# Kernel tuning notes

Measured on AMD Instinct MI355X. Metric: run time of the kernel, lower is better.

Reference implementation:

```python
import jax, jax.numpy as jnp
import numpy as np

DIM = 1792      # 256+512+1024 = WRN50 layer1-3 channels
GAMMA_D = 1
K_TOP = 3
EPS = 0.1
MAX_ITER = 200
B, H, W = 2, 56, 56


def avg_pool3x3(x):
    # F.avg_pool2d(x, 3, 1, 1), count_include_pad=True -> always divide by 9
    s = jax.lax.reduce_window(x, 0.0, jax.lax.add, (1, 1, 3, 3), (1, 1, 1, 1),
                              [(0, 0), (0, 0), (1, 1), (1, 1)])
    return s / 9.0


def descriptor(p1, p2, p3, w_coord, b_coord, w_eca):
    sample = avg_pool3x3(p1)
    b, _, h, w = sample.shape
    for o in (p2, p3):
        o = avg_pool3x3(o)
        # F.interpolate(..., mode='bilinear', align_corners=False) == half-pixel bilinear
        o = jax.image.resize(o, (o.shape[0], o.shape[1], h, w), method='bilinear')
        sample = jnp.concatenate([sample, o], axis=1)      # [b,1792,h,w]
    # CoordConv2d(dim, dim//gamma_d, 1): append normalized coord channels, 1x1 conv
    xx = jnp.broadcast_to(jnp.linspace(-1.0, 1.0, w, dtype=sample.dtype)[None, None, None, :], (b, 1, h, w))
    yy = jnp.broadcast_to(jnp.linspace(-1.0, 1.0, h, dtype=sample.dtype)[None, None, :, None], (b, 1, h, w))
    z = jnp.concatenate([sample, xx, yy], axis=1)          # [b,1794,h,w]
    phi = jnp.einsum('bchw,oc->bohw', z, w_coord) + b_coord[None, :, None, None]
    # eca_layer(dim, k_size=9): GAP -> conv1d over channel axis -> sigmoid gate
    y = phi.mean(axis=(2, 3))                              # [b,C]
    y = jax.lax.conv_general_dilated(y[:, None, :], w_eca[None, None, :], (1,),
                                     [(4, 4)], dimension_numbers=('NCH', 'OIH', 'NCH'))[:, 0, :]
    gate = jax.nn.sigmoid(y)[:, :, None, None]
    return phi * (1.0 + 0.1 * gate)                        # 0.1*eca(phi) + phi


def sinkhorn(Ccost, mu, nu):
    # plain Sinkhorn (TopK_custom forward), 200 iterations
    G = jnp.exp(-Ccost / EPS)                              # [bs,n,m]
    bs, n, m = Ccost.shape

    def body(i, uv):
        u, v = uv
        u = mu / (G * v).sum(-1, keepdims=True)            # [bs,n,1]
        v = nu / (G * u).sum(-2, keepdims=True)            # [bs,1,m]
        return (u, v)

    u0 = jnp.ones((bs, n, 1), Ccost.dtype)
    v0 = jnp.ones((bs, 1, m), Ccost.dtype) / m
    u, v = jax.lax.fori_loop(0, MAX_ITER, body, (u0, v0))
    return u * G * v


def soft_topk(scores):
    # SOFT top-k via 2-anchor optimal transport; selects the K_TOP SMALLEST scores
    bs, n = scores.shape
    anchors = jnp.array([0.0, 1.0], scores.dtype)          # [selected, rest]
    Ccost = (scores[..., None] - anchors) ** 2             # [bs,n,2]
    Ccost = Ccost / jax.lax.stop_gradient(Ccost.max())
    mu = jnp.ones((1, n, 1), scores.dtype) / n
    nu = jnp.array([K_TOP / n, (n - K_TOP) / n], scores.dtype).reshape(1, 1, 2)
    Gamma = sinkhorn(Ccost, mu, nu)
    return Gamma[..., 0] * n                               # soft top-K membership mask


def adfa_forward(p1, p2, p3, w_coord, b_coord, w_eca, C):
    phi = descriptor(p1, p2, p3, w_coord, b_coord, w_eca)  # [b,c,h,w]
    b, c, h, w = phi.shape
    phi_p = phi.reshape(b, c, h * w).transpose(0, 2, 1)    # [b,hw,c]
    # F.kl_div(log_softmax(phi_p), softmax(C^T)) = t*(log t - log q); summed, detached
    t = jax.nn.softmax(C.T, axis=-1)                       # [nC,c], nC == hw
    kl = t * (jnp.log(t) - jax.nn.log_softmax(phi_p, axis=-1))
    kldist = jax.lax.stop_gradient(kl.sum(axis=(1, 2), keepdims=True))  # [b,1,1]
    feat2 = (phi_p ** 2).sum(-1, keepdims=True)            # [b,hw,1]
    cent2 = (C ** 2).sum(0, keepdims=True)                 # [1,nC]
    dist = (feat2 + cent2 - 2.0 * (phi_p @ C)) * kldist    # [b,hw,nC]
    nC = dist.shape[-1]
    mask = soft_topk(dist.reshape(-1, nC)).reshape(dist.shape)
    d = (mask * dist).sum(-1, keepdims=True)               # [b,hw,1]
    # rearrange 'b (h w) c -> b c h w'
    return jnp.sqrt(d).reshape(b, h, w, 1).transpose(0, 3, 1, 2)  # [b,1,h,w]


def setup_inputs() -> dict:
    key = jax.random.key(0)
    ks = jax.random.split(key, 7)
    p1 = jax.random.normal(ks[0], (B, 256, H, W), jnp.float32)
    p2 = jax.random.normal(ks[1], (B, 512, H // 2, W // 2), jnp.float32)
    p3 = jax.random.normal(ks[2], (B, 1024, H // 4, W // 4), jnp.float32)
    fan_in = DIM + 2
    w_coord = jax.random.normal(ks[3], (DIM // GAMMA_D, fan_in), jnp.float32) / np.float32(np.sqrt(fan_in))
    b_coord = jax.random.normal(ks[4], (DIM // GAMMA_D,), jnp.float32) * 0.01
    w_eca = jax.random.normal(ks[5], (9,), jnp.float32) / 3.0
    C = jax.random.normal(ks[6], (DIM // GAMMA_D, H * W), jnp.float32) * 0.3
    return {"p1": p1, "p2": p2, "p3": p3, "w_coord": w_coord,
            "b_coord": b_coord, "w_eca": w_eca, "C": C}


def reference(p1, p2, p3, w_coord, b_coord, w_eca, C):
    return adfa_forward(p1, p2, p3, w_coord, b_coord, w_eca, C)
```

## Files before the change

kernel.cpp:

```cpp
#include <hip/hip_runtime.h>

#define HWn 3136
#define DIMc 1792
#define ZCc 1794
#define NBb 2
#define KP 1856
#define MP 3200

typedef unsigned short u16;
typedef unsigned int u32;
typedef short bf16x8 __attribute__((ext_vector_type(8)));
typedef float f32x4 __attribute__((ext_vector_type(4)));

#define GL_LDS(gp, lp) __builtin_amdgcn_global_load_lds(\
    (const __attribute__((address_space(1))) void*)(gp), \
    (__attribute__((address_space(3))) void*)(lp), 16, 0, 0)

__device__ __forceinline__ u16 f2b(float f) {
  u32 u = __float_as_uint(f);
  u32 r = (u + 0x7fffu + ((u >> 16) & 1u)) >> 16;
  return (u16)r;
}
__device__ __forceinline__ float b2f(u16 h) { return __uint_as_float((u32)h << 16); }

__device__ __forceinline__ int xcd_swz(int orig, int nwg) {
  int q = nwg >> 3, r = nwg & 7;
  int xcd = orig & 7, j = orig >> 3;
  int base = (xcd < r) ? xcd * (q + 1) : r * (q + 1) + (xcd - r) * q;
  return base + j;
}

__device__ __forceinline__ float blkSum256(float v) {
  __shared__ float sh[4];
  #pragma unroll
  for (int o = 32; o > 0; o >>= 1) v += __shfl_xor(v, o, 64);
  int lane = threadIdx.x & 63, w = threadIdx.x >> 6;
  if (lane == 0) sh[w] = v;
  __syncthreads();
  float r = sh[0] + sh[1] + sh[2] + sh[3];
  __syncthreads();
  return r;
}
__device__ __forceinline__ float blkMax256(float v) {
  __shared__ float sh[4];
  #pragma unroll
  for (int o = 32; o > 0; o >>= 1) v = fmaxf(v, __shfl_xor(v, o, 64));
  int lane = threadIdx.x & 63, w = threadIdx.x >> 6;
  if (lane == 0) sh[w] = v;
  __syncthreads();
  float r = fmaxf(fmaxf(sh[0], sh[1]), fmaxf(sh[2], sh[3]));
  __syncthreads();
  return r;
}
__device__ __forceinline__ float blkMin256(float v) {
  __shared__ float sh[4];
  #pragma unroll
  for (int o = 32; o > 0; o >>= 1) v = fminf(v, __shfl_xor(v, o, 64));
  int lane = threadIdx.x & 63, w = threadIdx.x >> 6;
  if (lane == 0) sh[w] = v;
  __syncthreads();
  float r = fminf(fminf(sh[0], sh[1]), fminf(sh[2], sh[3]));
  __syncthreads();
  return r;
}

__global__ void pool_k(const float* __restrict__ in, float* __restrict__ out,
                       int total, int Hh, int Ww) {
  int idx = blockIdx.x * 256 + threadIdx.x;
  if (idx >= total) return;
  int w = idx % Ww; int h = (idx / Ww) % Hh; int bc = idx / (Ww * Hh);
  const float* p = in + (size_t)bc * Hh * Ww;
  float s = 0.f;
  #pragma unroll
  for (int dy = -1; dy <= 1; dy++) {
    int y = h + dy; if ((unsigned)y >= (unsigned)Hh) continue;
    #pragma unroll
    for (int dx = -1; dx <= 1; dx++) {
      int x = w + dx; if ((unsigned)x >= (unsigned)Ww) continue;
      s += p[y * Ww + x];
    }
  }
  out[idx] = s * (1.f / 9.f);
}

__device__ __forceinline__ float bilerp(const float* __restrict__ p, int Hin, int Win,
                                        int h, int w, float sc) {
  float fy = (h + 0.5f) * sc - 0.5f;
  float fx = (w + 0.5f) * sc - 0.5f;
  float y0f = floorf(fy), x0f = floorf(fx);
  int y0 = (int)y0f, x0 = (int)x0f;
  float wy = fy - y0f, wx = fx - x0f;
  int y0c = min(max(y0, 0), Hin - 1);
  int y1c = min(max(y0 + 1, 0), Hin - 1);
  int x0c = min(max(x0, 0), Win - 1);
  int x1c = min(max(x0 + 1, 0), Win - 1);
  float v00 = p[y0c * Win + x0c], v01 = p[y0c * Win + x1c];
  float v10 = p[y1c * Win + x0c], v11 = p[y1c * Win + x1c];
  return (1.f - wy) * ((1.f - wx) * v00 + wx * v01) + wy * ((1.f - wx) * v10 + wx * v11);
}

__global__ __launch_bounds__(256) void buildzt_k(const float* __restrict__ p1,
    const float* __restrict__ pp2, const float* __restrict__ pp3,
    u16* __restrict__ zt, float* __restrict__ psum) {
  __shared__ u16 tile[64][68];
  int b = blockIdx.z;
  int i0 = blockIdx.x * 64;
  int c0 = blockIdx.y * 64;
  int t = threadIdx.x;
  #pragma unroll
  for (int q = 0; q < 16; q++) {
    int idx = q * 256 + t;
    int cp = idx >> 6, ip = idx & 63;
    int cg = c0 + cp;
    int ig = i0 + ip;
    int h = ig / 56, w = ig % 56;
    float val;
    if (cg < 256) {
      const float* p = p1 + (size_t)(b * 256 + cg) * HWn;
      float s = 0.f;
      #pragma unroll
      for (int dy = -1; dy <= 1; dy++) {
        int y = h + dy; if ((unsigned)y >= 56u) continue;
        #pragma unroll
        for (int dx = -1; dx <= 1; dx++) {
          int x = w + dx; if ((unsigned)x >= 56u) continue;
          s += p[y * 56 + x];
        }
      }
      val = s * (1.f / 9.f);
    } else if (cg < 768) {
      val = bilerp(pp2 + (size_t)(b * 512 + (cg - 256)) * 784, 28, 28, h, w, 0.5f);
    } else if (cg < 1792) {
      val = bilerp(pp3 + (size_t)(b * 1024 + (cg - 768)) * 196, 14, 14, h, w, 0.25f);
    } else if (cg == 1792) {
      val = -1.f + (2.f / 55.f) * (float)w;
    } else if (cg == 1793) {
      val = -1.f + (2.f / 55.f) * (float)h;
    } else {
      val = 0.f;
    }
    tile[cp][ip] = f2b(val);
  }
  __syncthreads();
  #pragma unroll
  for (int q = 0; q < 4; q++) {
    int idx = q * 256 + t;
    int r2 = idx >> 4;
    int cc4 = (idx & 15) * 4;
    u32 lo = (u32)tile[cc4 + 0][r2] | ((u32)tile[cc4 + 1][r2] << 16);
    u32 hi = (u32)tile[cc4 + 2][r2] | ((u32)tile[cc4 + 3][r2] << 16);
    *reinterpret_cast<uint2*>(&zt[((size_t)b * MP + i0 + r2) * KP + c0 + cc4]) = make_uint2(lo, hi);
  }
  if (t < 64) {
    float s = 0.f;
    #pragma unroll 8
    for (int j = 0; j < 64; j++) s += b2f(tile[t][j]);
    psum[(((size_t)b * 29 + blockIdx.y) * 49 + blockIdx.x) * 64 + t] = s;
  }
}

__global__ void zred_k(const float* __restrict__ psum, float* __restrict__ zmean) {
  int cty = blockIdx.x, b = blockIdx.y;
  int t = threadIdx.x;
  float s = 0.f;
  for (int ix = 0; ix < 49; ix++)
    s += psum[(((size_t)b * 29 + cty) * 49 + ix) * 64 + t];
  zmean[b * KP + cty * 64 + t] = s * (1.f / (float)HWn);
}

__global__ __launch_bounds__(256) void yv_k(const u16* __restrict__ Wb, const float* __restrict__ zmean,
                                            const float* __restrict__ bias, float* __restrict__ yv) {
  __shared__ float zs[KP];
  int b = blockIdx.y;
  int o0 = blockIdx.x * 16;
  int t = threadIdx.x;
  for (int k = t; k < KP; k += 256) zs[k] = zmean[b * KP + k];
  __syncthreads();
  int w = t >> 6, l = t & 63;
  #pragma unroll
  for (int q = 0; q < 4; q++) {
    int o = o0 + w * 4 + q;
    const u16* R = Wb + (size_t)o * KP;
    float s = 0.f;
    for (int base = l * 8; base < KP; base += 512) {
      bf16x8 v = *reinterpret_cast<const bf16x8*>(&R[base]);
      #pragma unroll
      for (int j = 0; j < 8; j++) s += b2f((u16)v[j]) * zs[base + j];
    }
    #pragma unroll
    for (int off = 32; off > 0; off >>= 1) s += __shfl_xor(s, off, 64);
    if (l == 0) yv[b * DIMc + o] = s + bias[o];
  }
}

__global__ __launch_bounds__(256) void transC_k(const float* __restrict__ src, u16* __restrict__ dst) {
  __shared__ u16 tile[64][68];
  int i0 = blockIdx.x * 64;
  int c0 = blockIdx.y * 64;
  int t = threadIdx.x;
  bool vi = (i0 < HWn);
  #pragma unroll
  for (int q = 0; q < 4; q++) {
    int idx = q * 256 + t;
    int r = idx >> 4;
    int c4 = (idx & 15) * 4;
    int sr = c0 + r;
    if (vi && sr < DIMc) {
      float4 rv = *reinterpret_cast<const float4*>(&src[(size_t)sr * HWn + i0 + c4]);
      tile[r][c4 + 0] = f2b(rv.x); tile[r][c4 + 1] = f2b(rv.y);
      tile[r][c4 + 2] = f2b(rv.z); tile[r][c4 + 3] = f2b(rv.w);
    } else {
      tile[r][c4 + 0] = 0; tile[r][c4 + 1] = 0; tile[r][c4 + 2] = 0; tile[r][c4 + 3] = 0;
    }
  }
  __syncthreads();
  #pragma unroll
  for (int q = 0; q < 4; q++) {
    int idx = q * 256 + t;
    int r2 = idx >> 4;
    int cc4 = (idx & 15) * 4;
    u32 lo = (u32)tile[cc4 + 0][r2] | ((u32)tile[cc4 + 1][r2] << 16);
    u32 hi = (u32)tile[cc4 + 2][r2] | ((u32)tile[cc4 + 3][r2] << 16);
    *reinterpret_cast<uint2*>(&dst[(size_t)(i0 + r2) * KP + c0 + cc4]) = make_uint2(lo, hi);
  }
}

__global__ void convW_k(const float* __restrict__ Wc, u16* __restrict__ Wb) {
  int idx = blockIdx.x * 256 + threadIdx.x;
  const int total = DIMc * KP;
  if (idx >= total) return;
  int k = idx % KP, m = idx / KP;
  Wb[idx] = (k < ZCc) ? f2b(Wc[(size_t)m * ZCc + k]) : (u16)0;
}

#define STAGEF(buf, koff) { _Pragma("unroll") for (int j = 0; j < 2; j++) { \
    GL_LDS(gA[j] + (koff), &lA[buf][(j * 256 + tid) * 8]); \
    GL_LDS(gB[j] + (koff), &lB[buf][(j * 256 + tid) * 8]); } }

template<int DIST>
__global__ __launch_bounds__(256, 5) void gemmF_k(
    const u16* __restrict__ A, const u16* __restrict__ B,
    int ntN, int NT,
    const float* __restrict__ bias, u16* __restrict__ PhiOut,
    const float* __restrict__ feat2, const float* __restrict__ cent2,
    const float* __restrict__ kld, float* __restrict__ Dist,
    float* __restrict__ mmpart, int nblk) {
  __shared__ u16 lA[2][128 * 32];
  __shared__ u16 lB[2][128 * 32];
  int tid = threadIdx.x;
  int wid = tid >> 6, lane = tid & 63;
  int wm = wid >> 1, wn = wid & 1;
  int orig = blockIdx.x;
  int wg = xcd_swz(orig, gridDim.x);
  int mt = wg / ntN, nt = wg % ntN;
  int m0 = mt * 128, n0 = nt * 128;
  int rbase = tid >> 2;
  int srcX = ((tid & 3) ^ ((rbase >> 1) & 3)) * 8;
  const u16* gA[2]; const u16* gB[2];
  #pragma unroll
  for (int j = 0; j < 2; j++) {
    int rr = j * 64 + rbase;
    gA[j] = A + (size_t)(m0 + rr) * KP + srcX;
    gB[j] = B + (size_t)(n0 + rr) * KP + srcX;
  }
  int kq8 = (lane >> 4) * 8;
  int lr = lane & 15;
  f32x4 acc[4][4] = {};
  STAGEF(0, 0);
  __syncthreads();
  for (int t = 0; t < NT; t++) {
    int cur = t & 1;
    if (t + 1 < NT) STAGEF(cur ^ 1, (t + 1) * 32);
    bf16x8 af[4], bfr[4];
    #pragma unroll
    for (int f = 0; f < 4; f++) {
      int aR = wm * 64 + f * 16 + lr;
      af[f] = *reinterpret_cast<const bf16x8*>(
          &lA[cur][aR * 32 + (kq8 ^ (((aR >> 1) & 3) << 3))]);
    }
    #pragma unroll
    for (int g = 0; g < 4; g++) {
      int bR = wn * 64 + g * 16 + lr;
      bfr[g] = *reinterpret_cast<const bf16x8*>(
          &lB[cur][bR * 32 + (kq8 ^ (((bR >> 1) & 3) << 3))]);
    }
    #pragma unroll
    for (int f = 0; f < 4; f++)
      #pragma unroll
      for (int g = 0; g < 4; g++)
        acc[f][g] = __builtin_amdgcn_mfma_f32_16x16x32_bf16(af[f], bfr[g], acc[f][g], 0, 0, 0);
    __syncthreads();
  }
  int mbase = m0 + wm * 64 + (lane >> 4) * 4;
  int nbase = n0 + wn * 64 + lr;
  if (DIST == 0) {
    #pragma unroll
    for (int mi = 0; mi < 4; mi++) {
      #pragma unroll
      for (int ni = 0; ni < 4; ni++) {
        int n = nbase + ni * 16;
        float bv = bias[n];
        #pragma unroll
        for (int r = 0; r < 4; r++) {
          int m = mbase + mi * 16 + r;
          PhiOut[(size_t)m * KP + n] = f2b(acc[mi][ni][r] + bv);
        }
      }
    }
  } else {
    float lmin = 3.4e38f, lmax = -3.4e38f;
    #pragma unroll
    for (int mi = 0; mi < 4; mi++) {
      int m = mbase + mi * 16;
      int bz = m / MP;
      int i = m - bz * MP;
      float kl = kld[bz];
      float f2r[4];
      #pragma unroll
      for (int r = 0; r < 4; r++)
        f2r[r] = (i + r < HWn) ? feat2[bz * HWn + i + r] : 0.f;
      #pragma unroll
      for (int ni = 0; ni < 4; ni++) {
        int n = nbase + ni * 16;
        if (n < HWn) {
          float c2 = cent2[n];
          #pragma unroll
          for (int r = 0; r < 4; r++) {
            if (i + r < HWn) {
              float dd = (f2r[r] + c2 - 2.f * acc[mi][ni][r]) * kl;
              Dist[((size_t)bz * HWn + i + r) * HWn + n] = dd;
              lmin = fminf(lmin, dd); lmax = fmaxf(lmax, dd);
            }
          }
        }
      }
    }
    #pragma unroll
    for (int o = 32; o > 0; o >>= 1) {
      lmin = fminf(lmin, __shfl_xor(lmin, o, 64));
      lmax = fmaxf(lmax, __shfl_xor(lmax, o, 64));
    }
    __syncthreads();
    float* scr = reinterpret_cast<float*>(&lA[0][0]);
    if (lane == 0) { scr[wid] = lmin; scr[4 + wid] = lmax; }
    __syncthreads();
    if (tid == 0) {
      mmpart[orig] = fminf(fminf(scr[0], scr[1]), fminf(scr[2], scr[3]));
      mmpart[nblk + orig] = fmaxf(fmaxf(scr[4], scr[5]), fmaxf(scr[6], scr[7]));
    }
  }
}

__global__ void fac_k(const float* __restrict__ yv, const float* __restrict__ weca,
                      float* __restrict__ fac) {
  int idx = blockIdx.x * 256 + threadIdx.x;
  if (idx >= NBb * DIMc) return;
  int o = idx % DIMc; int b = idx / DIMc;
  float s = 0.f;
  #pragma unroll
  for (int k = 0; k < 9; k++) {
    int c = o + k - 4;
    if ((unsigned)c < (unsigned)DIMc) s += yv[b * DIMc + c] * weca[k];
  }
  fac[idx] = 1.f + 0.1f / (1.f + expf(-s));
}

__global__ __launch_bounds__(256) void rowfuse_k(const u16* __restrict__ Ct, u16* __restrict__ Phi,
    const float* __restrict__ fac, float* __restrict__ cent2,
    float* __restrict__ feat2, float* __restrict__ kpart) {
  int i = blockIdx.x;
  int t = threadIdx.x;
  bool act = (t * 8 < DIMc);
  const u16* R = Ct + (size_t)i * KP;
  float c[8];
  float mc = -3.4e38f, c2 = 0.f;
  if (act) {
    bf16x8 x = *reinterpret_cast<const bf16x8*>(&R[t * 8]);
    #pragma unroll
    for (int j = 0; j < 8; j++) {
      c[j] = b2f((u16)x[j]);
      mc = fmaxf(mc, c[j]);
      c2 += c[j] * c[j];
    }
  }
  mc = blkMax256(mc);
  float se = 0.f, sce = 0.f;
  float e[8];
  if (act) {
    #pragma unroll
    for (int j = 0; j < 8; j++) {
      e[j] = expf(c[j] - mc);
      se += e[j]; sce += e[j] * (c[j] - mc);
    }
  }
  se = blkSum256(se);
  sce = blkSum256(sce);
  c2 = blkSum256(c2);
  if (t == 0) cent2[i] = c2;
  float tl = sce / se - logf(se);
  float inv_se = 1.f / se;
  #pragma unroll
  for (int b = 0; b < NBb; b++) {
    u16* P = Phi + (size_t)b * MP * KP + (size_t)i * KP;
    float v[8];
    float mx = -3.4e38f;
    if (act) {
      bf16x8 x = *reinterpret_cast<const bf16x8*>(&P[t * 8]);
      const float4* fp = reinterpret_cast<const float4*>(&fac[b * DIMc + t * 8]);
      float4 f0 = fp[0], f1 = fp[1];
      v[0] = b2f((u16)x[0]) * f0.x; v[1] = b2f((u16)x[1]) * f0.y;
      v[2] = b2f((u16)x[2]) * f0.z; v[3] = b2f((u16)x[3]) * f0.w;
      v[4] = b2f((u16)x[4]) * f1.x; v[5] = b2f((u16)x[5]) * f1.y;
      v[6] = b2f((u16)x[6]) * f1.z; v[7] = b2f((u16)x[7]) * f1.w;
      #pragma unroll
      for (int j = 0; j < 8; j++) mx = fmaxf(mx, v[j]);
    }
    mx = blkMax256(mx);
    float sp = 0.f, f2 = 0.f, td = 0.f;
    if (act) {
      bf16x8 o;
      #pragma unroll
      for (int j = 0; j < 8; j++) {
        sp += expf(v[j] - mx);
        f2 += v[j] * v[j];
        td += e[j] * v[j];
        o[j] = (short)f2b(v[j]);
      }
      *reinterpret_cast<bf16x8*>(&P[t * 8]) = o;
    } else if (t * 8 < KP) {
      bf16x8 zr = {};
      *reinterpret_cast<bf16x8*>(&P[t * 8]) = zr;
    }
    sp = blkSum256(sp);
    f2 = blkSum256(f2);
    td = blkSum256(td);
    if (t == 0) {
      feat2[b * HWn + i] = f2;
      kpart[b * HWn + i] = tl - td * inv_se + (mx + logf(sp));
    }
  }
}

__global__ __launch_bounds__(256) void kldred_k(const float* __restrict__ kpart, float* __restrict__ kld) {
  float s0 = 0.f, s1 = 0.f;
  for (int i = threadIdx.x; i < HWn; i += 256) { s0 += kpart[i]; s1 += kpart[HWn + i]; }
  s0 = blkSum256(s0); s1 = blkSum256(s1);
  if (threadIdx.x == 0) { kld[0] = s0; kld[1] = s1; }
}

__global__ __launch_bounds__(256) void mmred_k(const float* __restrict__ mmpart, float* __restrict__ gmm,
                                               int nblk) {
  float lmin = 3.4e38f, lmax = -3.4e38f;
  for (int i = threadIdx.x; i < nblk; i += 256) {
    lmin = fminf(lmin, mmpart[i]);
    lmax = fmaxf(lmax, mmpart[nblk + i]);
  }
  lmin = blkMin256(lmin); lmax = blkMax256(lmax);
  if (threadIdx.x == 0) { gmm[0] = lmin; gmm[1] = lmax; }
}

__global__ __launch_bounds__(256) void topk_k(const float* __restrict__ dist,
    const float* __restrict__ gmm, float* __restrict__ out) {
  __shared__ float dS[HWn];
  __shared__ float rS[HWn];
  int row = blockIdx.x;
  const float* dr = dist + (size_t)row * HWn;
  int t = threadIdx.x;
  float gmin = gmm[0], gmax = gmm[1];
  float cmax = fmaxf(fmaxf(gmin * gmin, (gmin - 1.f) * (gmin - 1.f)),
                     fmaxf(gmax * gmax, (gmax - 1.f) * (gmax - 1.f)));
  float inv = 1.f / (0.1f * cmax);
  for (int ch = t; ch < HWn / 4; ch += 256) {
    float4 d4 = *reinterpret_cast<const float4*>(&dr[ch * 4]);
    dS[ch * 4 + 0] = d4.x; rS[ch * 4 + 0] = expf((2.f * d4.x - 1.f) * inv);
    dS[ch * 4 + 1] = d4.y; rS[ch * 4 + 1] = expf((2.f * d4.y - 1.f) * inv);
    dS[ch * 4 + 2] = d4.z; rS[ch * 4 + 2] = expf((2.f * d4.z - 1.f) * inv);
    dS[ch * 4 + 3] = d4.w; rS[ch * 4 + 3] = expf((2.f * d4.w - 1.f) * inv);
  }
  __syncthreads();
  const float nf = (float)HWn;
  float s = 1.f;
  for (int it = 0; it < 199; it++) {
    float loc = 0.f;
    for (int e = t; e < HWn; e += 256) loc += 1.f / (1.f + rS[e] * s);
    float A = blkSum256(loc);
    float snew = ((nf - 3.f) / 3.f) * A * s / fmaxf(nf - A, 1e-20f);
    float ds = fabsf(snew - s);
    s = snew;
    if (ds <= 1e-6f * fabsf(s)) break;
  }
  float loc = 0.f;
  for (int e = t; e < HWn; e += 256) loc += 1.f / (1.f + rS[e] * s);
  float A = blkSum256(loc);
  float sc = 3.f / A;
  float dl = 0.f;
  for (int e = t; e < HWn; e += 256) dl += dS[e] / (1.f + rS[e] * s);
  float dsum = blkSum256(dl) * sc;
  if (t == 0) out[row] = sqrtf(fmaxf(dsum, 0.f));
}

extern "C" void kernel_launch(void* const* d_in, const int* in_sizes, int n_in,
                              void* d_out, int out_size, void* d_ws, size_t ws_size,
                              hipStream_t stream) {
  const float* p1 = (const float*)d_in[0];
  const float* p2 = (const float*)d_in[1];
  const float* p3 = (const float*)d_in[2];
  const float* wcoord = (const float*)d_in[3];
  const float* bcoord = (const float*)d_in[4];
  const float* weca = (const float*)d_in[5];
  const float* Cm = (const float*)d_in[6];
  float* out = (float*)d_out;
  float* ws = (float*)d_ws;

  u16*   zt    = (u16*)ws;
  float* pp2   = ws + 5939200;
  float* pp3   = ws + 6742016;
  float* dist  = ws;
  u16*   phi   = (u16*)(ws + 19668992);
  u16*   Ct    = (u16*)(ws + 25608192);
  u16*   Wb    = (u16*)(ws + 28577792);
  float* yv    = ws + 30240768;
  float* fac   = yv + 3584;
  float* feat2 = fac + 3584;
  float* cent2 = feat2 + 6272;
  float* kpart = cent2 + 3136;
  float* kld   = kpart + 6272;
  float* mmpart= kld + 2;
  float* gmm   = mmpart + 2500;
  float* zmean = gmm + 2;
  float* psum  = zmean + 3712;
  const int NBLK = 50 * 25;

  pool_k<<<3136, 256, 0, stream>>>(p2, pp2, NBb * 512 * 784, 28, 28);
  pool_k<<<1568, 256, 0, stream>>>(p3, pp3, NBb * 1024 * 196, 14, 14);
  buildzt_k<<<dim3(49, 29, NBb), 256, 0, stream>>>(p1, pp2, pp3, zt, psum);
  zred_k<<<dim3(29, NBb), 64, 0, stream>>>(psum, zmean);
  convW_k<<<(DIMc * KP + 255) / 256, 256, 0, stream>>>(wcoord, Wb);
  transC_k<<<dim3(50, 29, 1), 256, 0, stream>>>(Cm, Ct);
  yv_k<<<dim3(DIMc / 16, NBb), 256, 0, stream>>>(Wb, zmean, bcoord, yv);
  fac_k<<<(NBb * DIMc + 255) / 256, 256, 0, stream>>>(yv, weca, fac);
  gemmF_k<0><<<50 * 14, 256, 0, stream>>>(
      zt, Wb, 14, 58, bcoord, phi,
      nullptr, nullptr, nullptr, nullptr, nullptr, 0);
  rowfuse_k<<<HWn, 256, 0, stream>>>(Ct, phi, fac, cent2, feat2, kpart);
  kldred_k<<<1, 256, 0, stream>>>(kpart, kld);
  gemmF_k<1><<<50 * 25, 256, 0, stream>>>(
      phi, Ct, 25, 56, nullptr, nullptr,
      feat2, cent2, kld, dist, mmpart, NBLK);
  mmred_k<<<1, 256, 0, stream>>>(mmpart, gmm, NBLK);
  topk_k<<<NBb * HWn, 256, 0, stream>>>(dist, gmm, out);
}
```

Before: 324.3 us.

## Store distance matrix in bf16 and overlap GEMM loads with single-barrier pipelining

The large distance matrix (2x3136x3136) written by the GEMM epilogue and re-read by the top-k kernel is now stored as bf16 rather than fp32, halving that round-trip traffic. The top-k kernel loads 8 bf16 values per thread and converts them to float. The GEMM main loop also swaps the trailing __syncthreads for raw barriers plus explicit vmcnt waits, so the next tile's global-to-LDS load is issued before the current tile's MFMAs. Rounding distances to bf16 loses precision in the soft top-k input, which can shift the output and accuracy.

```diff
diff --git a/kernel.cpp b/kernel.cpp
--- a/kernel.cpp
+++ b/kernel.cpp
@@ -15,6 +15,9 @@
 #define GL_LDS(gp, lp) __builtin_amdgcn_global_load_lds(\
     (const __attribute__((address_space(1))) void*)(gp), \
     (__attribute__((address_space(3))) void*)(lp), 16, 0, 0)
+
+#define WAITVM(N) asm volatile("s_waitcnt vmcnt(" #N ")" ::: "memory")
+#define BARRIER_RAW() asm volatile("s_barrier" ::: "memory")
 
 __device__ __forceinline__ u16 f2b(float f) {
   u32 u = __float_as_uint(f);
@@ -243,7 +246,7 @@
     int ntN, int NT,
     const float* __restrict__ bias, u16* __restrict__ PhiOut,
     const float* __restrict__ feat2, const float* __restrict__ cent2,
-    const float* __restrict__ kld, float* __restrict__ Dist,
+    const float* __restrict__ kld, u16* __restrict__ DistB,
     float* __restrict__ mmpart, int nblk) {
   __shared__ u16 lA[2][128 * 32];
   __shared__ u16 lB[2][128 * 32];
@@ -267,10 +270,12 @@
   int lr = lane & 15;
   f32x4 acc[4][4] = {};
   STAGEF(0, 0);
-  __syncthreads();
   for (int t = 0; t < NT; t++) {
     int cur = t & 1;
-    if (t + 1 < NT) STAGEF(cur ^ 1, (t + 1) * 32);
+    BARRIER_RAW();
+    if (t + 1 < NT) { STAGEF(cur ^ 1, (t + 1) * 32); WAITVM(4); }
+    else WAITVM(0);
+    BARRIER_RAW();
     bf16x8 af[4], bfr[4];
     #pragma unroll
     for (int f = 0; f < 4; f++) {
@@ -289,7 +294,6 @@
       #pragma unroll
       for (int g = 0; g < 4; g++)
         acc[f][g] = __builtin_amdgcn_mfma_f32_16x16x32_bf16(af[f], bfr[g], acc[f][g], 0, 0, 0);
-    __syncthreads();
   }
   int mbase = m0 + wm * 64 + (lane >> 4) * 4;
   int nbase = n0 + wn * 64 + lr;
@@ -328,7 +332,7 @@
           for (int r = 0; r < 4; r++) {
             if (i + r < HWn) {
               float dd = (f2r[r] + c2 - 2.f * acc[mi][ni][r]) * kl;
-              Dist[((size_t)bz * HWn + i + r) * HWn + n] = dd;
+              DistB[((size_t)bz * HWn + i + r) * HWn + n] = f2b(dd);
               lmin = fminf(lmin, dd); lmax = fmaxf(lmax, dd);
             }
           }
@@ -459,23 +463,25 @@
   if (threadIdx.x == 0) { gmm[0] = lmin; gmm[1] = lmax; }
 }
 
-__global__ __launch_bounds__(256) void topk_k(const float* __restrict__ dist,
+__global__ __launch_bounds__(256) void topk_k(const u16* __restrict__ dist,
     const float* __restrict__ gmm, float* __restrict__ out) {
   __shared__ float dS[HWn];
   __shared__ float rS[HWn];
   int row = blockIdx.x;
-  const float* dr = dist + (size_t)row * HWn;
+  const u16* dr = dist + (size_t)row * HWn;
   int t = threadIdx.x;
   float gmin = gmm[0], gmax = gmm[1];
   float cmax = fmaxf(fmaxf(gmin * gmin, (gmin - 1.f) * (gmin - 1.f)),
                      fmaxf(gmax * gmax, (gmax - 1.f) * (gmax - 1.f)));
   float inv = 1.f / (0.1f * cmax);
-  for (int ch = t; ch < HWn / 4; ch += 256) {
-    float4 d4 = *reinterpret_cast<const float4*>(&dr[ch * 4]);
-    dS[ch * 4 + 0] = d4.x; rS[ch * 4 + 0] = expf((2.f * d4.x - 1.f) * inv);
-    dS[ch * 4 + 1] = d4.y; rS[ch * 4 + 1] = expf((2.f * d4.y - 1.f) * inv);
-    dS[ch * 4 + 2] = d4.z; rS[ch * 4 + 2] = expf((2.f * d4.z - 1.f) * inv);
-    dS[ch * 4 + 3] = d4.w; rS[ch * 4 + 3] = expf((2.f * d4.w - 1.f) * inv);
+  for (int ch = t; ch < HWn / 8; ch += 256) {
+    bf16x8 d8 = *reinterpret_cast<const bf16x8*>(&dr[ch * 8]);
+    #pragma unroll
+    for (int j = 0; j < 8; j++) {
+      float dv = b2f((u16)d8[j]);
+      dS[ch * 8 + j] = dv;
+      rS[ch * 8 + j] = expf((2.f * dv - 1.f) * inv);
+    }
   }
   __syncthreads();
   const float nf = (float)HWn;
@@ -515,7 +521,7 @@
   u16*   zt    = (u16*)ws;
   float* pp2   = ws + 5939200;
   float* pp3   = ws + 6742016;
-  float* dist  = ws;
+  u16*   dist  = (u16*)ws;
   u16*   phi   = (u16*)(ws + 19668992);
   u16*   Ct    = (u16*)(ws + 25608192);
   u16*   Wb    = (u16*)(ws + 28577792);
```

New measurement: 333.0 us. 2.7% more time.
